# Performance work log

Measured on AMD Instinct MI355X. Metric: run time of the kernel, lower is better.

## Reference

```python
import jax, jax.numpy as jnp
import numpy as np

B, N, C_IN, C_OUT = 8, 4096, 64, 64
NEG_INF = -9e15
LEAKY_SLOPE = 0.01  # torch F.leaky_relu default


def setup_inputs() -> dict:
    key = jax.random.key(0)
    kx, ka, kw, kq, kk = jax.random.split(key, 5)
    X = jax.random.normal(kx, (B, N, C_IN), dtype=jnp.float32)
    A = jax.random.randint(ka, (N, N), 0, 2, dtype=jnp.int32)
    # xavier_uniform with gain=1.414 ~ scaled uniform; plain scaled normal is fine for a numeric reference
    def xavier(k, shape):
        fan_in, fan_out = shape
        bound = 1.414 * np.sqrt(6.0 / (fan_in + fan_out))
        return jax.random.uniform(k, shape, jnp.float32, -bound, bound)
    weight = xavier(kw, (C_IN, C_OUT))
    query = xavier(kq, (C_IN, C_OUT))
    key_p = xavier(kk, (C_IN, C_OUT))
    return {"X": X, "A": A, "weight": weight, "query": query, "key_p": key_p}


def reference(X, A, weight, query, key_p):
    n = X.shape[1]
    idx = jnp.arange(n)
    adj = A.at[idx, idx].set(1)  # add self-loops
    out = jnp.einsum('bni,io->bno', X, weight)
    q = jnp.einsum('bni,io->bno', X, query)
    k = jnp.einsum('bni,io->bno', X, key_p)
    att = jnp.einsum('bnd,bmd->bnm', q, k)          # QK^T, (B,N,N)
    att = jax.nn.leaky_relu(att, LEAKY_SLOPE)
    att = jnp.where(adj[None, :, :] > 0, att, NEG_INF)
    att = jax.nn.softmax(att, axis=-1)
    # dropout p=0 and/or eval mode -> identity
    return jnp.einsum('bnm,bmo->bno', att, out)
```

## Files before the change

kernel.cpp:

```cpp
#include <hip/hip_runtime.h>
#include <stdint.h>

#define BATCH 8
#define NN 4096
#define CC 64
#define MASKV -1.0e30f
#define LOG2E 1.4426950408889634f

typedef _Float16 half8 __attribute__((ext_vector_type(8)));
typedef __fp16 fp16x2 __attribute__((ext_vector_type(2)));
typedef float f32x4 __attribute__((ext_vector_type(4)));

__global__ __launch_bounds__(256) void gat_proj(
    const float* __restrict__ X, const float* __restrict__ W0,
    const float* __restrict__ Wq, const float* __restrict__ Wk,
    _Float16* __restrict__ qh, _Float16* __restrict__ ql,
    _Float16* __restrict__ kb, _Float16* __restrict__ vt)
{
    __shared__ alignas(16) _Float16 WTh[3][64][72];
    __shared__ alignas(16) _Float16 WTl[3][64][72];
    const int t = threadIdx.x;
    const float* Ws[3] = {W0, Wq, Wk};
    for (int e = t; e < 4096; e += 256) {
        int k = e >> 6, c = e & 63;
        #pragma unroll
        for (int m = 0; m < 3; ++m) {
            float w = Ws[m][e];
            _Float16 hi = (_Float16)w;
            WTh[m][c][k] = hi;
            WTl[m][c][k] = (_Float16)(w - (float)hi);
        }
    }
    __syncthreads();
    const int lane = t & 63, wv = t >> 6;
    const int cl = lane & 15, g = lane >> 4;
    {
        int tile = blockIdx.x * 4 + wv;
        int gr = tile * 16;
        const float* xr = X + (size_t)(gr + cl) * CC;
        half8 xh[2], xl[2];
        #pragma unroll
        for (int kf = 0; kf < 2; ++kf) {
            f32x4 a0 = *(const f32x4*)(xr + g*8 + kf*32);
            f32x4 a1 = *(const f32x4*)(xr + g*8 + kf*32 + 4);
            half8 h, l;
            #pragma unroll
            for (int j = 0; j < 4; ++j) {
                _Float16 h0 = (_Float16)a0[j], h1 = (_Float16)a1[j];
                h[j]   = h0; l[j]   = (_Float16)(a0[j] - (float)h0);
                h[j+4] = h1; l[j+4] = (_Float16)(a1[j] - (float)h1);
            }
            xh[kf] = h; xl[kf] = l;
        }
        #pragma unroll
        for (int mat = 1; mat <= 2; ++mat) {
            #pragma unroll
            for (int nt = 0; nt < 4; ++nt) {
                f32x4 acc = {0.f, 0.f, 0.f, 0.f};
                #pragma unroll
                for (int kf = 0; kf < 2; ++kf) {
                    half8 bh = *(const half8*)&WTh[mat][nt*16 + cl][g*8 + kf*32];
                    half8 bl = *(const half8*)&WTl[mat][nt*16 + cl][g*8 + kf*32];
                    acc = __builtin_amdgcn_mfma_f32_16x16x32_f16(xh[kf], bh, acc, 0, 0, 0);
                    acc = __builtin_amdgcn_mfma_f32_16x16x32_f16(xl[kf], bh, acc, 0, 0, 0);
                    acc = __builtin_amdgcn_mfma_f32_16x16x32_f16(xh[kf], bl, acc, 0, 0, 0);
                }
                #pragma unroll
                for (int i = 0; i < 4; ++i) {
                    size_t off = (size_t)(gr + 4*g + i) * CC + nt*16 + cl;
                    if (mat == 1) {
                        float qs = acc[i] * LOG2E;
                        _Float16 hi = (_Float16)qs;
                        qh[off] = hi;
                        ql[off] = (_Float16)(qs - (float)hi);
                    } else {
                        kb[off] = (_Float16)acc[i];
                    }
                }
            }
        }
        {
            int b = gr >> 12, n0 = gr & (NN - 1);
            #pragma unroll
            for (int mt = 0; mt < 4; ++mt) {
                f32x4 acc = {0.f, 0.f, 0.f, 0.f};
                #pragma unroll
                for (int kf = 0; kf < 2; ++kf) {
                    half8 ah = *(const half8*)&WTh[0][mt*16 + cl][g*8 + kf*32];
                    half8 al = *(const half8*)&WTl[0][mt*16 + cl][g*8 + kf*32];
                    acc = __builtin_amdgcn_mfma_f32_16x16x32_f16(ah, xh[kf], acc, 0, 0, 0);
                    acc = __builtin_amdgcn_mfma_f32_16x16x32_f16(al, xh[kf], acc, 0, 0, 0);
                    acc = __builtin_amdgcn_mfma_f32_16x16x32_f16(ah, xl[kf], acc, 0, 0, 0);
                }
                #pragma unroll
                for (int i = 0; i < 4; ++i) {
                    int co = mt*16 + 4*g + i;
                    vt[((size_t)b * CC + co) * NN + n0 + cl] = (_Float16)acc[i];
                }
            }
        }
    }
}

__global__ __launch_bounds__(256) void gat_mask(const int* __restrict__ A,
                                                unsigned short* __restrict__ M16)
{
    const int row = blockIdx.x;
    const int w16 = threadIdx.x;
    const int4* ap = (const int4*)(A + (size_t)row * NN + w16 * 16);
    unsigned m = 0;
    #pragma unroll
    for (int j = 0; j < 4; ++j) {
        int4 a = ap[j];
        m |= (a.x != 0 ? 1u : 0u) << (4*j);
        m |= (a.y != 0 ? 1u : 0u) << (4*j + 1);
        m |= (a.z != 0 ? 1u : 0u) << (4*j + 2);
        m |= (a.w != 0 ? 1u : 0u) << (4*j + 3);
    }
    if (w16 == (row >> 4)) m |= 1u << (row & 15);
    M16[(size_t)row * 256 + w16] = (unsigned short)m;
}

__global__ __launch_bounds__(256) void gat_attn(
    const _Float16* __restrict__ qh, const _Float16* __restrict__ ql,
    const _Float16* __restrict__ kf16, const _Float16* __restrict__ vtb,
    const unsigned long long* __restrict__ M,
    _Float16* __restrict__ po, float2* __restrict__ pml)
{
    __shared__ alignas(16) _Float16 Kt[64][72];
    __shared__ alignas(16) _Float16 Vt[64][72];
    __shared__ alignas(16) _Float16 Ps[4][32][72];
    const int t = threadIdx.x;
    const int lane = t & 63, wv = t >> 6;
    const int cl = lane & 15, g = lane >> 4;
    const int blk = blockIdx.x;
    const int b  = blk & 7;
    const int sp = (blk >> 3) & 3;
    const int qb = blk >> 5;
    const int Q0 = qb * 128 + wv * 32;
    const int c0 = sp * 16;

    half8 qfh[2][2], qfl[2][2];
    #pragma unroll
    for (int qt = 0; qt < 2; ++qt) {
        const _Float16* qrh = qh + ((size_t)b * NN + Q0 + qt*16 + cl) * CC;
        const _Float16* qrl = ql + ((size_t)b * NN + Q0 + qt*16 + cl) * CC;
        qfh[qt][0] = *(const half8*)(qrh + g*8);
        qfh[qt][1] = *(const half8*)(qrh + g*8 + 32);
        qfl[qt][0] = *(const half8*)(qrl + g*8);
        qfl[qt][1] = *(const half8*)(qrl + g*8 + 32);
    }
    const _Float16* kg = kf16 + (size_t)b * NN * CC;
    const _Float16* vg = vtb + (size_t)b * CC * NN;

    f32x4 o[2][4] = {};
    float m_run[2] = {MASKV, MASKV}, l_run[2] = {0.f, 0.f};

    uint4 pk0, pk1, pv0, pv1;
    unsigned long long pmA, pmB;
    auto loadchunk = [&](int kc) {
        const uint4* ks = (const uint4*)(kg + (size_t)kc * 64 * CC);
        pk0 = ks[t];
        pk1 = ks[t + 256];
        const _Float16* vs = vg + kc * 64;
        pv0 = *(const uint4*)(vs + (size_t)(t >> 3) * NN + (t & 7) * 8);
        pv1 = *(const uint4*)(vs + (size_t)((t >> 3) + 32) * NN + (t & 7) * 8);
        pmA = M[(size_t)(Q0 + cl) * 64 + kc];
        pmB = M[(size_t)(Q0 + 16 + cl) * 64 + kc];
    };
    loadchunk(c0);

    for (int kc = 0; kc < 16; ++kc) {
        __syncthreads();
        *(uint4*)&Kt[t >> 3][(t & 7) * 8] = pk0;
        *(uint4*)&Kt[(t >> 3) + 32][(t & 7) * 8] = pk1;
        *(uint4*)&Vt[t >> 3][(t & 7) * 8] = pv0;
        *(uint4*)&Vt[(t >> 3) + 32][(t & 7) * 8] = pv1;
        const unsigned long long cmA = pmA, cmB = pmB;
        __syncthreads();
        if (kc < 15) loadchunk(c0 + kc + 1);

        f32x4 sc[2][4] = {};
        #pragma unroll
        for (int kt = 0; kt < 4; ++kt) {
            #pragma unroll
            for (int kf = 0; kf < 2; ++kf) {
                half8 ka = *(const half8*)&Kt[kt*16 + cl][g*8 + kf*32];
                sc[0][kt] = __builtin_amdgcn_mfma_f32_16x16x32_f16(ka, qfh[0][kf], sc[0][kt], 0, 0, 0);
                sc[0][kt] = __builtin_amdgcn_mfma_f32_16x16x32_f16(ka, qfl[0][kf], sc[0][kt], 0, 0, 0);
                sc[1][kt] = __builtin_amdgcn_mfma_f32_16x16x32_f16(ka, qfh[1][kf], sc[1][kt], 0, 0, 0);
                sc[1][kt] = __builtin_amdgcn_mfma_f32_16x16x32_f16(ka, qfl[1][kf], sc[1][kt], 0, 0, 0);
            }
        }

        #pragma unroll
        for (int qt = 0; qt < 2; ++qt) {
            const unsigned long long cm = qt ? cmB : cmA;
            const unsigned mwx = (unsigned)cm, mwy = (unsigned)(cm >> 32);
            float sv[16];
            float mx = MASKV;
            #pragma unroll
            for (int kt = 0; kt < 4; ++kt) {
                unsigned wmw = (kt < 2) ? mwx : mwy;
                #pragma unroll
                for (int i = 0; i < 4; ++i) {
                    float x = sc[qt][kt][i];
                    x = fmaxf(x, 0.01f * x);
                    int bit = ((kt & 1) * 16) + 4*g + i;
                    x = ((wmw >> bit) & 1u) ? x : MASKV;
                    sv[kt*4 + i] = x;
                    mx = fmaxf(mx, x);
                }
            }
            mx = fmaxf(mx, __shfl_xor(mx, 16));
            mx = fmaxf(mx, __shfl_xor(mx, 32));
            if (__any(mx > m_run[qt])) {
                float nm = fmaxf(m_run[qt], mx);
                float alpha = __builtin_amdgcn_exp2f(m_run[qt] - nm);
                m_run[qt] = nm;
                l_run[qt] *= alpha;
                #pragma unroll
                for (int ct = 0; ct < 4; ++ct) o[qt][ct] *= alpha;
            }
            float lsum = 0.f;
            float p[16];
            #pragma unroll
            for (int j = 0; j < 16; ++j) {
                p[j] = __builtin_amdgcn_exp2f(sv[j] - m_run[qt]);
                lsum += p[j];
            }
            l_run[qt] += lsum;
            #pragma unroll
            for (int kt = 0; kt < 4; ++kt) {
                union { fp16x2 h; unsigned u; } p0u, p1u;
                p0u.h = __builtin_amdgcn_cvt_pkrtz(p[kt*4+0], p[kt*4+1]);
                p1u.h = __builtin_amdgcn_cvt_pkrtz(p[kt*4+2], p[kt*4+3]);
                uint2 pw = {p0u.u, p1u.u};
                *(uint2*)&Ps[wv][qt*16 + cl][kt*16 + 4*g] = pw;
            }
        }
        __builtin_amdgcn_wave_barrier();

        half8 pf[2][2];
        #pragma unroll
        for (int qt = 0; qt < 2; ++qt) {
            pf[qt][0] = *(const half8*)&Ps[wv][qt*16 + cl][g*8];
            pf[qt][1] = *(const half8*)&Ps[wv][qt*16 + cl][g*8 + 32];
        }
        #pragma unroll
        for (int ct = 0; ct < 4; ++ct) {
            half8 vf0 = *(const half8*)&Vt[ct*16 + cl][g*8];
            half8 vf1 = *(const half8*)&Vt[ct*16 + cl][g*8 + 32];
            #pragma unroll
            for (int qt = 0; qt < 2; ++qt) {
                o[qt][ct] = __builtin_amdgcn_mfma_f32_16x16x32_f16(vf0, pf[qt][0], o[qt][ct], 0, 0, 0);
                o[qt][ct] = __builtin_amdgcn_mfma_f32_16x16x32_f16(vf1, pf[qt][1], o[qt][ct], 0, 0, 0);
            }
        }
    }

    #pragma unroll
    for (int qt = 0; qt < 2; ++qt) {
        float lt = l_run[qt];
        lt += __shfl_xor(lt, 16);
        lt += __shfl_xor(lt, 32);
        size_t base = (size_t)sp * (BATCH * NN) + (size_t)b * NN + Q0 + qt*16 + cl;
        _Float16* orow = po + base * 64;
        #pragma unroll
        for (int ct = 0; ct < 4; ++ct) {
            union { fp16x2 h; unsigned u; } o0u, o1u;
            o0u.h = __builtin_amdgcn_cvt_pkrtz(o[qt][ct][0], o[qt][ct][1]);
            o1u.h = __builtin_amdgcn_cvt_pkrtz(o[qt][ct][2], o[qt][ct][3]);
            uint2 ow = {o0u.u, o1u.u};
            *(uint2*)(orow + ct*16 + 4*g) = ow;
        }
        if (g == 0) pml[base] = make_float2(m_run[qt], lt);
    }
}

__global__ __launch_bounds__(256) void gat_comb(
    const _Float16* __restrict__ po, const float2* __restrict__ pml,
    float* __restrict__ out)
{
    int gid = blockIdx.x * 256 + threadIdx.x;
    int row = gid >> 2;
    int col = (gid & 3) * 16;
    float2 ml[4];
    float Mx = MASKV;
    #pragma unroll
    for (int s = 0; s < 4; ++s) {
        ml[s] = pml[s * (BATCH * NN) + row];
        Mx = fmaxf(Mx, ml[s].x);
    }
    float w[4], den = 0.f;
    #pragma unroll
    for (int s = 0; s < 4; ++s) {
        w[s] = __builtin_amdgcn_exp2f(ml[s].x - Mx);
        den += w[s] * ml[s].y;
    }
    float inv = 1.0f / den;
    float acc[16] = {};
    #pragma unroll
    for (int s = 0; s < 4; ++s) {
        const _Float16* p = po + ((size_t)s * (BATCH * NN) + row) * 64 + col;
        float a = w[s] * inv;
        half8 v0 = *(const half8*)(p);
        half8 v1 = *(const half8*)(p + 8);
        #pragma unroll
        for (int j = 0; j < 8; ++j) {
            acc[j]     += a * (float)v0[j];
            acc[j + 8] += a * (float)v1[j];
        }
    }
    float* op = out + (size_t)row * 64 + col;
    #pragma unroll
    for (int i = 0; i < 4; ++i) {
        f32x4 r = {acc[4*i], acc[4*i+1], acc[4*i+2], acc[4*i+3]};
        *(f32x4*)(op + i*4) = r;
    }
}

extern "C" void kernel_launch(void* const* d_in, const int* in_sizes, int n_in,
                              void* d_out, int out_size, void* d_ws, size_t ws_size,
                              hipStream_t stream) {
    const float* X  = (const float*)d_in[0];
    const int*   A  = (const int*)d_in[1];
    const float* W0 = (const float*)d_in[2];
    const float* Wq = (const float*)d_in[3];
    const float* Wk = (const float*)d_in[4];
    float* out = (float*)d_out;
    char* ws = (char*)d_ws;
    const size_t SZ = (size_t)BATCH * NN * CC * 2;
    _Float16* qh  = (_Float16*)(ws);
    _Float16* ql  = (_Float16*)(ws + SZ);
    _Float16* kbf = (_Float16*)(ws + 2*SZ);
    _Float16* vtb = (_Float16*)(ws + 3*SZ);
    char* Mbase = ws + 4*SZ;
    _Float16* po = (_Float16*)(Mbase + 2*1024*1024);
    float2* pml  = (float2*)(Mbase + 2*1024*1024 + 4*SZ);

    hipLaunchKernelGGL(gat_proj, dim3(512),  dim3(256), 0, stream, X, W0, Wq, Wk, qh, ql, kbf, vtb);
    hipLaunchKernelGGL(gat_mask, dim3(4096), dim3(256), 0, stream, A, (unsigned short*)Mbase);
    hipLaunchKernelGGL(gat_attn, dim3(1024), dim3(256), 0, stream, qh, ql, kbf, vtb,
                       (const unsigned long long*)Mbase, po, pml);
    hipLaunchKernelGGL(gat_comb, dim3(512),  dim3(256), 0, stream, po, pml, out);
}
```

Before: 207.1 us.

## Double-buffer K/V tiles, pass P via ds_bpermute, merge proj and mask kernels

The attention kernel now double-buffers the K and V shared-memory tiles, so each chunk loop needs one barrier instead of two, and the next tile's global loads and stores overlap the current compute. The probability tile moves from the softmax output layout into the MFMA B-operand layout with ds_bpermute cross-lane shuffles instead of a shared-memory round trip, which removes the Ps buffer. The projection and mask-packing kernels are merged into one launch by branching on block index, saving a kernel launch. The cost is more shared memory for the K/V buffers, more registers for the prefetched chunk and masks, and extra permute instructions.

Result: slower. 214.0 us (+3.4%).

```diff
diff --git a/kernel.cpp b/kernel.cpp
--- a/kernel.cpp
+++ b/kernel.cpp
@@ -11,15 +11,33 @@
 typedef __fp16 fp16x2 __attribute__((ext_vector_type(2)));
 typedef float f32x4 __attribute__((ext_vector_type(4)));
 
-__global__ __launch_bounds__(256) void gat_proj(
+__global__ __launch_bounds__(256) void gat_prep(
     const float* __restrict__ X, const float* __restrict__ W0,
     const float* __restrict__ Wq, const float* __restrict__ Wk,
+    const int* __restrict__ A,
     _Float16* __restrict__ qh, _Float16* __restrict__ ql,
-    _Float16* __restrict__ kb, _Float16* __restrict__ vt)
+    _Float16* __restrict__ kb, _Float16* __restrict__ vt,
+    unsigned short* __restrict__ M16)
 {
     __shared__ alignas(16) _Float16 WTh[3][64][72];
     __shared__ alignas(16) _Float16 WTl[3][64][72];
     const int t = threadIdx.x;
+    if (blockIdx.x >= 512) {
+        const int row = blockIdx.x - 512;
+        const int4* ap = (const int4*)(A + (size_t)row * NN + t * 16);
+        unsigned m = 0;
+        #pragma unroll
+        for (int j = 0; j < 4; ++j) {
+            int4 a = ap[j];
+            m |= (a.x != 0 ? 1u : 0u) << (4*j);
+            m |= (a.y != 0 ? 1u : 0u) << (4*j + 1);
+            m |= (a.z != 0 ? 1u : 0u) << (4*j + 2);
+            m |= (a.w != 0 ? 1u : 0u) << (4*j + 3);
+        }
+        if (t == (row >> 4)) m |= 1u << (row & 15);
+        M16[(size_t)row * 256 + t] = (unsigned short)m;
+        return;
+    }
     const float* Ws[3] = {W0, Wq, Wk};
     for (int e = t; e < 4096; e += 256) {
         int k = e >> 6, c = e & 63;
@@ -102,34 +120,14 @@
     }
 }
 
-__global__ __launch_bounds__(256) void gat_mask(const int* __restrict__ A,
-                                                unsigned short* __restrict__ M16)
-{
-    const int row = blockIdx.x;
-    const int w16 = threadIdx.x;
-    const int4* ap = (const int4*)(A + (size_t)row * NN + w16 * 16);
-    unsigned m = 0;
-    #pragma unroll
-    for (int j = 0; j < 4; ++j) {
-        int4 a = ap[j];
-        m |= (a.x != 0 ? 1u : 0u) << (4*j);
-        m |= (a.y != 0 ? 1u : 0u) << (4*j + 1);
-        m |= (a.z != 0 ? 1u : 0u) << (4*j + 2);
-        m |= (a.w != 0 ? 1u : 0u) << (4*j + 3);
-    }
-    if (w16 == (row >> 4)) m |= 1u << (row & 15);
-    M16[(size_t)row * 256 + w16] = (unsigned short)m;
-}
-
 __global__ __launch_bounds__(256) void gat_attn(
     const _Float16* __restrict__ qh, const _Float16* __restrict__ ql,
     const _Float16* __restrict__ kf16, const _Float16* __restrict__ vtb,
     const unsigned long long* __restrict__ M,
     _Float16* __restrict__ po, float2* __restrict__ pml)
 {
-    __shared__ alignas(16) _Float16 Kt[64][72];
-    __shared__ alignas(16) _Float16 Vt[64][72];
-    __shared__ alignas(16) _Float16 Ps[4][32][72];
+    __shared__ alignas(16) _Float16 Kt[2][64][72];
+    __shared__ alignas(16) _Float16 Vt[2][64][72];
     const int t = threadIdx.x;
     const int lane = t & 63, wv = t >> 6;
     const int cl = lane & 15, g = lane >> 4;
@@ -152,6 +150,9 @@
     }
     const _Float16* kg = kf16 + (size_t)b * NN * CC;
     const _Float16* vg = vtb + (size_t)b * CC * NN;
+
+    const int addrA = 4 * (cl + 32 * (g & 1));
+    const int addrB = addrA + 64;
 
     f32x4 o[2][4] = {};
     float m_run[2] = {MASKV, MASKV}, l_run[2] = {0.f, 0.f};
@@ -168,24 +169,29 @@
         pmA = M[(size_t)(Q0 + cl) * 64 + kc];
         pmB = M[(size_t)(Q0 + 16 + cl) * 64 + kc];
     };
+    auto storebuf = [&](int bu) {
+        *(uint4*)&Kt[bu][t >> 3][(t & 7) * 8] = pk0;
+        *(uint4*)&Kt[bu][(t >> 3) + 32][(t & 7) * 8] = pk1;
+        *(uint4*)&Vt[bu][t >> 3][(t & 7) * 8] = pv0;
+        *(uint4*)&Vt[bu][(t >> 3) + 32][(t & 7) * 8] = pv1;
+    };
+
     loadchunk(c0);
+    storebuf(0);
+    unsigned long long cmA = pmA, cmB = pmB;
+    loadchunk(c0 + 1);
+    unsigned long long nmA = pmA, nmB = pmB;
+    __syncthreads();
 
     for (int kc = 0; kc < 16; ++kc) {
-        __syncthreads();
-        *(uint4*)&Kt[t >> 3][(t & 7) * 8] = pk0;
-        *(uint4*)&Kt[(t >> 3) + 32][(t & 7) * 8] = pk1;
-        *(uint4*)&Vt[t >> 3][(t & 7) * 8] = pv0;
-        *(uint4*)&Vt[(t >> 3) + 32][(t & 7) * 8] = pv1;
-        const unsigned long long cmA = pmA, cmB = pmB;
-        __syncthreads();
-        if (kc < 15) loadchunk(c0 + kc + 1);
+        const int cur = kc & 1;
 
         f32x4 sc[2][4] = {};
         #pragma unroll
         for (int kt = 0; kt < 4; ++kt) {
             #pragma unroll
             for (int kf = 0; kf < 2; ++kf) {
-                half8 ka = *(const half8*)&Kt[kt*16 + cl][g*8 + kf*32];
+                half8 ka = *(const half8*)&Kt[cur][kt*16 + cl][g*8 + kf*32];
                 sc[0][kt] = __builtin_amdgcn_mfma_f32_16x16x32_f16(ka, qfh[0][kf], sc[0][kt], 0, 0, 0);
                 sc[0][kt] = __builtin_amdgcn_mfma_f32_16x16x32_f16(ka, qfl[0][kf], sc[0][kt], 0, 0, 0);
                 sc[1][kt] = __builtin_amdgcn_mfma_f32_16x16x32_f16(ka, qfh[1][kf], sc[1][kt], 0, 0, 0);
@@ -193,6 +199,10 @@
             }
         }
 
+        if (kc < 15) storebuf(cur ^ 1);
+        if (kc < 14) loadchunk(c0 + kc + 2);
+
+        half8 pfq[2][2];
         #pragma unroll
         for (int qt = 0; qt < 2; ++qt) {
             const unsigned long long cm = qt ? cmB : cmA;
@@ -230,33 +240,46 @@
                 lsum += p[j];
             }
             l_run[qt] += lsum;
+            unsigned p2[8];
             #pragma unroll
             for (int kt = 0; kt < 4; ++kt) {
-                union { fp16x2 h; unsigned u; } p0u, p1u;
-                p0u.h = __builtin_amdgcn_cvt_pkrtz(p[kt*4+0], p[kt*4+1]);
-                p1u.h = __builtin_amdgcn_cvt_pkrtz(p[kt*4+2], p[kt*4+3]);
-                uint2 pw = {p0u.u, p1u.u};
-                *(uint2*)&Ps[wv][qt*16 + cl][kt*16 + 4*g] = pw;
-            }
-        }
-        __builtin_amdgcn_wave_barrier();
-
-        half8 pf[2][2];
-        #pragma unroll
-        for (int qt = 0; qt < 2; ++qt) {
-            pf[qt][0] = *(const half8*)&Ps[wv][qt*16 + cl][g*8];
-            pf[qt][1] = *(const half8*)&Ps[wv][qt*16 + cl][g*8 + 32];
-        }
+                union { fp16x2 h; unsigned u; } c0u, c1u;
+                c0u.h = __builtin_amdgcn_cvt_pkrtz(p[kt*4+0], p[kt*4+1]);
+                c1u.h = __builtin_amdgcn_cvt_pkrtz(p[kt*4+2], p[kt*4+3]);
+                p2[kt*2]     = c0u.u;
+                p2[kt*2 + 1] = c1u.u;
+            }
+            const bool ghi = (g & 2) != 0;
+            #pragma unroll
+            for (int f = 0; f < 2; ++f) {
+                unsigned RA[4], RB[4];
+                #pragma unroll
+                for (int P = 0; P < 4; ++P) {
+                    RA[P] = (unsigned)__builtin_amdgcn_ds_bpermute(addrA, (int)p2[4*f + P]);
+                    RB[P] = (unsigned)__builtin_amdgcn_ds_bpermute(addrB, (int)p2[4*f + P]);
+                }
+                union { unsigned u[4]; half8 h; } bf;
+                bf.u[0] = ghi ? RA[2] : RA[0];
+                bf.u[1] = ghi ? RA[3] : RA[1];
+                bf.u[2] = ghi ? RB[2] : RB[0];
+                bf.u[3] = ghi ? RB[3] : RB[1];
+                pfq[qt][f] = bf.h;
+            }
+        }
+
         #pragma unroll
         for (int ct = 0; ct < 4; ++ct) {
-            half8 vf0 = *(const half8*)&Vt[ct*16 + cl][g*8];
-            half8 vf1 = *(const half8*)&Vt[ct*16 + cl][g*8 + 32];
+            half8 vf0 = *(const half8*)&Vt[cur][ct*16 + cl][g*8];
+            half8 vf1 = *(const half8*)&Vt[cur][ct*16 + cl][g*8 + 32];
             #pragma unroll
             for (int qt = 0; qt < 2; ++qt) {
-                o[qt][ct] = __builtin_amdgcn_mfma_f32_16x16x32_f16(vf0, pf[qt][0], o[qt][ct], 0, 0, 0);
-                o[qt][ct] = __builtin_amdgcn_mfma_f32_16x16x32_f16(vf1, pf[qt][1], o[qt][ct], 0, 0, 0);
-            }
-        }
+                o[qt][ct] = __builtin_amdgcn_mfma_f32_16x16x32_f16(vf0, pfq[qt][0], o[qt][ct], 0, 0, 0);
+                o[qt][ct] = __builtin_amdgcn_mfma_f32_16x16x32_f16(vf1, pfq[qt][1], o[qt][ct], 0, 0, 0);
+            }
+        }
+        cmA = nmA; cmB = nmB;
+        nmA = pmA; nmB = pmB;
+        __syncthreads();
     }
 
     #pragma unroll
@@ -339,8 +362,8 @@
     _Float16* po = (_Float16*)(Mbase + 2*1024*1024);
     float2* pml  = (float2*)(Mbase + 2*1024*1024 + 4*SZ);
 
-    hipLaunchKernelGGL(gat_proj, dim3(512),  dim3(256), 0, stream, X, W0, Wq, Wk, qh, ql, kbf, vtb);
-    hipLaunchKernelGGL(gat_mask, dim3(4096), dim3(256), 0, stream, A, (unsigned short*)Mbase);
+    hipLaunchKernelGGL(gat_prep, dim3(4608), dim3(256), 0, stream,
+                       X, W0, Wq, Wk, A, qh, ql, kbf, vtb, (unsigned short*)Mbase);
     hipLaunchKernelGGL(gat_attn, dim3(1024), dim3(256), 0, stream, qh, ql, kbf, vtb,
                        (const unsigned long long*)Mbase, po, pml);
     hipLaunchKernelGGL(gat_comb, dim3(512),  dim3(256), 0, stream, po, pml, out);
```
